# Kernel optimization log

Hardware: AMD Instinct MI355X
Metric: run time of the kernel (lower is better)

The kernel has to match this reference:

```python
import jax, jax.numpy as jnp
import numpy as np

EMBED_DIM = 1024
NUM_HEADS = 16
HEAD_DIM = EMBED_DIM // NUM_HEADS


def setup_inputs() -> dict:
    key = jax.random.key(0)
    ks = jax.random.split(key, 6)
    B, S = 2, 2048
    x = jax.random.normal(ks[0], (B, S, EMBED_DIM), dtype=jnp.float32)
    # causal boolean mask, broadcast to (B, H, S, S)
    causal = jnp.tril(jnp.ones((S, S), dtype=bool))
    mask = jnp.broadcast_to(causal, (B, NUM_HEADS, S, S))
    s_in = 1.0 / np.sqrt(EMBED_DIM)
    qkv_w = jax.random.normal(ks[1], (3 * EMBED_DIM, EMBED_DIM), dtype=jnp.float32) * s_in
    qkv_b = jax.random.normal(ks[2], (3 * EMBED_DIM,), dtype=jnp.float32) * 0.01
    proj_w = jax.random.normal(ks[3], (EMBED_DIM, EMBED_DIM), dtype=jnp.float32) * s_in
    proj_b = jax.random.normal(ks[4], (EMBED_DIM,), dtype=jnp.float32) * 0.01
    return {"x": x, "mask": mask, "qkv_w": qkv_w, "qkv_b": qkv_b,
            "proj_w": proj_w, "proj_b": proj_b}


def reference(x, mask, qkv_w, qkv_b, proj_w, proj_b):
    B, S, E = x.shape
    H, D = NUM_HEADS, HEAD_DIM
    qkv = x @ qkv_w.T + qkv_b                     # (B, S, 3E)
    q, k, v = jnp.split(qkv, 3, axis=-1)
    # (B, H, S, D)
    q = q.reshape(B, S, H, D).transpose(0, 2, 1, 3)
    k = k.reshape(B, S, H, D).transpose(0, 2, 1, 3)
    v = v.reshape(B, S, H, D).transpose(0, 2, 1, 3)
    scale = D ** (-0.5)
    attn = jnp.einsum('bhqd,bhkd->bhqk', q, k) * scale
    attn = jnp.where(mask, attn, jnp.float32(-10000.0))
    attn = attn - jnp.max(attn, axis=-1, keepdims=True)
    attn = jax.nn.softmax(attn, axis=-1)
    attn = jnp.where(mask, attn, jnp.float32(0.0))
    # dropout is identity in eval mode
    out = jnp.einsum('bhqk,bhkd->bhqd', attn, v)
    out = out.transpose(0, 2, 1, 3).reshape(B, S, E)
    return out @ proj_w.T + proj_b
```

## Files before the change

### kernel.cpp

```cpp
#include <hip/hip_runtime.h>
#include <hip/hip_bf16.h>

#define BATCH 2
#define SEQ 2048
#define EMBED 1024
#define NHEADS 16
#define HDIM 64

typedef __hip_bfloat16 bf16;
typedef __attribute__((ext_vector_type(8))) short bf16x8;
typedef __attribute__((ext_vector_type(4))) short bf16x4;
typedef __attribute__((ext_vector_type(4))) float f32x4;

typedef const __attribute__((address_space(1))) void* gaddr_t;
typedef __attribute__((address_space(3))) void* laddr_t;

__device__ __forceinline__ bf16x8 lds_frag8(const bf16* p) {
    const bf16x4 a = *(const bf16x4*)p;
    const bf16x4 b = *(const bf16x4*)(p + 4);
    return __builtin_shufflevector(a, b, 0, 1, 2, 3, 4, 5, 6, 7);
}

__global__ __launch_bounds__(256)
void f2b_all(const float* __restrict__ s0, bf16* __restrict__ d0, int n0,
             const float* __restrict__ s1, bf16* __restrict__ d1, int n1,
             const float* __restrict__ s2, bf16* __restrict__ d2, int n2)
{
    int i = blockIdx.x * 256 + threadIdx.x;
    const float* s; bf16* d;
    if (i < n0)                { s = s0; d = d0; }
    else if ((i -= n0) < n1)   { s = s1; d = d1; }
    else if ((i -= n1) < n2)   { s = s2; d = d2; }
    else return;
    const float4 v = ((const float4*)s)[i];
    union { ushort4 u4; bf16 h[4]; } o;
    o.h[0] = __float2bfloat16(v.x);
    o.h[1] = __float2bfloat16(v.y);
    o.h[2] = __float2bfloat16(v.z);
    o.h[3] = __float2bfloat16(v.w);
    ((ushort4*)d)[i] = o.u4;
}

template<int MODE>
__global__ __launch_bounds__(256)
void gemm_bt(const bf16* __restrict__ A, const bf16* __restrict__ B,
             const float* __restrict__ bias, void* __restrict__ Cv,
             int M, int N, int K)
{
    __shared__ __align__(16) bf16 lA[128 * 32];
    __shared__ __align__(16) bf16 lB[128 * 32];
    const int tid  = threadIdx.x;
    const int bn   = blockIdx.x, bm = blockIdx.y;
    const int wave = tid >> 6, lane = tid & 63;
    const int wm   = (wave >> 1) << 6, wn = (wave & 1) << 6;
    const int quad = lane >> 4, l16 = lane & 15;

    f32x4 acc[4][4] = {};

    for (int kt = 0; kt < K; kt += 32) {
        __syncthreads();
        #pragma unroll
        for (int i = 0; i < 2; ++i) {
            const int c = tid + (i << 8);
            const int r = c >> 2, kc = (c & 3) << 3;
            const bf16* gA = A + (long)(bm * 128 + r) * K + (kt + kc);
            const bf16* gB = B + (long)(bn * 128 + r) * K + (kt + kc);
            __builtin_amdgcn_global_load_lds((gaddr_t)gA, (laddr_t)&lA[c << 3], 16, 0, 0);
            __builtin_amdgcn_global_load_lds((gaddr_t)gB, (laddr_t)&lB[c << 3], 16, 0, 0);
        }
        __syncthreads();

        bf16x8 af[4], bfr[4];
        #pragma unroll
        for (int t = 0; t < 4; ++t) {
            af[t]  = *(const bf16x8*)&lA[(wm + t * 16 + l16) * 32 + quad * 8];
            bfr[t] = *(const bf16x8*)&lB[(wn + t * 16 + l16) * 32 + quad * 8];
        }
        #pragma unroll
        for (int tm = 0; tm < 4; ++tm)
            #pragma unroll
            for (int tn = 0; tn < 4; ++tn)
                acc[tm][tn] = __builtin_amdgcn_mfma_f32_16x16x32_bf16(
                    af[tm], bfr[tn], acc[tm][tn], 0, 0, 0);
    }

    #pragma unroll
    for (int tm = 0; tm < 4; ++tm) {
        #pragma unroll
        for (int tn = 0; tn < 4; ++tn) {
            const int gn = bn * 128 + wn + tn * 16 + l16;
            const float bv = bias[gn];
            if (MODE == 0) {
                #pragma unroll
                for (int r = 0; r < 4; ++r) {
                    const int gm = bm * 128 + wm + tm * 16 + quad * 4 + r;
                    ((float*)Cv)[(long)gm * N + gn] = acc[tm][tn][r] + bv;
                }
            } else {
                const int part = gn >> 10, h = (gn >> 6) & (NHEADS - 1), d = gn & (HDIM - 1);
                const int gm0 = bm * 128 + wm + tm * 16 + quad * 4;
                const int b = gm0 >> 11, s0 = gm0 & (SEQ - 1);
                if (part == 2) {
                    union { ushort4 u4; bf16 hv[4]; } o;
                    #pragma unroll
                    for (int r = 0; r < 4; ++r) o.hv[r] = __float2bfloat16(acc[tm][tn][r] + bv);
                    const long off = ((((long)2 * BATCH + b) * NHEADS + h) * HDIM + d) * SEQ + s0;
                    *(ushort4*)((bf16*)Cv + off) = o.u4;
                } else {
                    #pragma unroll
                    for (int r = 0; r < 4; ++r) {
                        const long off = ((((long)part * BATCH + b) * NHEADS + h) * SEQ + (s0 + r)) * HDIM + d;
                        ((bf16*)Cv)[off] = __float2bfloat16(acc[tm][tn][r] + bv);
                    }
                }
            }
        }
    }
}

__global__ __launch_bounds__(256)
void attn_nf(const bf16* __restrict__ Q, const bf16* __restrict__ K,
             const bf16* __restrict__ Vt, float* __restrict__ Op,
             float* __restrict__ lp)
{
    __shared__ __align__(16) bf16 pS[4 * 32 * 68];

    const int tid  = threadIdx.x;
    const int wave = tid >> 6, lane = tid & 63;
    const int quad = lane >> 4, l15 = lane & 15;
    const int bh   = blockIdx.x;
    const int half = blockIdx.y >> 4;
    const int qidx = blockIdx.y & 15;
    const int qg   = (15 - qidx) * 4 + wave;
    const int qw0  = qg * 32;

    const bf16* Qb  = Q  + (long)bh * SEQ * HDIM;
    const bf16* Kb  = K  + (long)bh * SEQ * HDIM;
    const bf16* Vtb = Vt + (long)bh * HDIM * SEQ;
    bf16* pW = pS + wave * 32 * 68;

    bf16x8 qf[2][2];
    #pragma unroll
    for (int mt = 0; mt < 2; ++mt)
        #pragma unroll
        for (int c = 0; c < 2; ++c) {
            union { int4 i; bf16x8 v; } u;
            u.i = *(const int4*)(Qb + (long)(qw0 + mt * 16 + l15) * HDIM + c * 32 + quad * 8);
            qf[mt][c] = u.v;
        }

    f32x4 acc[2][4] = {};
    float lsum[8] = {};

    const int nkt = (qw0 >> 6) + 1;
    const float sc = 0.125f * 1.44269504088896340736f;

    for (int t = half; t < nkt; t += 2) {
        const int kb = t * 64;

        f32x4 s[2][4] = {};
        #pragma unroll
        for (int c = 0; c < 2; ++c) {
            #pragma unroll
            for (int nt = 0; nt < 4; ++nt) {
                union { int4 i; bf16x8 v; } u;
                u.i = *(const int4*)(Kb + (long)(kb + nt * 16 + l15) * HDIM + c * 32 + quad * 8);
                #pragma unroll
                for (int mt = 0; mt < 2; ++mt)
                    s[mt][nt] = __builtin_amdgcn_mfma_f32_16x16x32_bf16(
                        qf[mt][c], u.v, s[mt][nt], 0, 0, 0);
            }
        }

        #pragma unroll
        for (int mt = 0; mt < 2; ++mt)
            #pragma unroll
            for (int nt = 0; nt < 4; ++nt)
                #pragma unroll
                for (int r = 0; r < 4; ++r) {
                    const int rl = mt * 16 + quad * 4 + r;
                    const int cl = nt * 16 + l15;
                    const float p = ((kb + cl) <= (qw0 + rl))
                        ? __builtin_amdgcn_exp2f(s[mt][nt][r] * sc) : 0.f;
                    lsum[mt * 4 + r] += p;
                    pW[rl * 68 + cl] = __float2bfloat16(p);
                }

        #pragma unroll
        for (int c = 0; c < 2; ++c) {
            bf16x8 pf[2];
            #pragma unroll
            for (int mt = 0; mt < 2; ++mt)
                pf[mt] = lds_frag8(&pW[(mt * 16 + l15) * 68 + c * 32 + quad * 8]);
            #pragma unroll
            for (int nt = 0; nt < 4; ++nt) {
                union { int4 i; bf16x8 v; } u;
                u.i = *(const int4*)(Vtb + (long)(nt * 16 + l15) * SEQ + kb + c * 32 + quad * 8);
                #pragma unroll
                for (int mt = 0; mt < 2; ++mt)
                    acc[mt][nt] = __builtin_amdgcn_mfma_f32_16x16x32_bf16(
                        pf[mt], u.v, acc[mt][nt], 0, 0, 0);
            }
        }
    }

    #pragma unroll
    for (int i = 0; i < 8; ++i)
        #pragma unroll
        for (int m = 1; m < 16; m <<= 1) lsum[i] += __shfl_xor(lsum[i], m, 64);

    const long halfO = (long)BATCH * NHEADS * SEQ * HDIM;
    float* Oh = Op + half * halfO + ((long)bh * SEQ) * HDIM;
    float* lh = lp + half * (BATCH * NHEADS * SEQ) + bh * SEQ;
    #pragma unroll
    for (int mt = 0; mt < 2; ++mt)
        #pragma unroll
        for (int r = 0; r < 4; ++r) {
            const int rl = mt * 16 + quad * 4 + r;
            float* orow = Oh + (long)(qw0 + rl) * HDIM;
            #pragma unroll
            for (int nt = 0; nt < 4; ++nt)
                orow[nt * 16 + l15] = acc[mt][nt][r];
            if (l15 == 0) lh[qw0 + rl] = lsum[mt * 4 + r];
        }
}

__global__ __launch_bounds__(256)
void attn_combine(const float* __restrict__ Op, const float* __restrict__ lp,
                  bf16* __restrict__ att)
{
    const int i = blockIdx.x * 256 + threadIdx.x;
    const int d4 = i & 15, q = (i >> 4) & (SEQ - 1), bh = i >> 15;
    const long halfO = (long)BATCH * NHEADS * SEQ * HDIM;
    const long rowo  = ((long)bh * SEQ + q) * HDIM;
    const float4 a = ((const float4*)(Op + rowo))[d4];
    const float4 b = ((const float4*)(Op + halfO + rowo))[d4];
    const int li = bh * SEQ + q;
    const float inv = 1.f / (lp[li] + lp[BATCH * NHEADS * SEQ + li]);
    const int bb = bh >> 4, h = bh & 15;
    union { ushort4 u4; bf16 hv[4]; } o;
    o.hv[0] = __float2bfloat16((a.x + b.x) * inv);
    o.hv[1] = __float2bfloat16((a.y + b.y) * inv);
    o.hv[2] = __float2bfloat16((a.z + b.z) * inv);
    o.hv[3] = __float2bfloat16((a.w + b.w) * inv);
    *(ushort4*)(att + ((long)bb * SEQ + q) * EMBED + h * HDIM + d4 * 4) = o.u4;
}

extern "C" void kernel_launch(void* const* d_in, const int* in_sizes, int n_in,
                              void* d_out, int out_size, void* d_ws, size_t ws_size,
                              hipStream_t stream)
{
    const float* x      = (const float*)d_in[0];
    const float* qkv_w  = (const float*)d_in[2];
    const float* qkv_b  = (const float*)d_in[3];
    const float* proj_w = (const float*)d_in[4];
    const float* proj_b = (const float*)d_in[5];
    float* out = (float*)d_out;

    const long nX  = (long)BATCH * SEQ * EMBED;
    const long nQW = 3L * EMBED * EMBED;
    const long nPW = (long)EMBED * EMBED;
    const long per = (long)BATCH * NHEADS * SEQ * HDIM;

    bf16* xw  = (bf16*)d_ws;
    bf16* qwm = xw + nX;
    bf16* pwm = qwm + nQW;
    bf16* qw  = pwm + nPW;
    bf16* kw  = qw + per;
    bf16* vw  = kw + per;
    bf16* att = vw + per;
    float* Op = (float*)(att + per);
    float* lp = Op + 2 * per;

    const int n0 = (int)(nX / 4), n1 = (int)(nQW / 4), n2 = (int)(nPW / 4);
    f2b_all<<<(n0 + n1 + n2 + 255) / 256, 256, 0, stream>>>(
        x, xw, n0, qkv_w, qwm, n1, proj_w, pwm, n2);

    gemm_bt<1><<<dim3(3 * EMBED / 128, BATCH * SEQ / 128), 256, 0, stream>>>(
        xw, qwm, qkv_b, qw, BATCH * SEQ, 3 * EMBED, EMBED);

    attn_nf<<<dim3(BATCH * NHEADS, 32), 256, 0, stream>>>(qw, kw, vw, Op, lp);
    attn_combine<<<(int)(per / 4 / 256), 256, 0, stream>>>(Op, lp, att);

    gemm_bt<0><<<dim3(EMBED / 128, BATCH * SEQ / 128), 256, 0, stream>>>(
        att, pwm, proj_b, out, BATCH * SEQ, EMBED, EMBED);
}
```

Before: 725.4 us.

## Transpose attention score MFMA, vectorize P stores, skip off-diagonal masking, narrow proj GEMM tile

The attention kernel now computes S transposed (K as the A operand), so each lane holds four consecutive keys for one query row. That lets P be written to LDS as 8-byte vector stores with a padded stride of 72 and read back as aligned 16-byte loads. The row-sum reduction shrinks to two shuffles, and causal masking is applied only on the diagonal tile. MFMA sections are wrapped in s_setprio. Separately, the output projection GEMM is templated to a 64-wide N tile, doubling its block count to improve occupancy on a small grid.

```diff
diff --git a/kernel.cpp b/kernel.cpp
--- a/kernel.cpp
+++ b/kernel.cpp
@@ -9,17 +9,10 @@
 
 typedef __hip_bfloat16 bf16;
 typedef __attribute__((ext_vector_type(8))) short bf16x8;
-typedef __attribute__((ext_vector_type(4))) short bf16x4;
 typedef __attribute__((ext_vector_type(4))) float f32x4;
 
 typedef const __attribute__((address_space(1))) void* gaddr_t;
 typedef __attribute__((address_space(3))) void* laddr_t;
-
-__device__ __forceinline__ bf16x8 lds_frag8(const bf16* p) {
-    const bf16x4 a = *(const bf16x4*)p;
-    const bf16x4 b = *(const bf16x4*)(p + 4);
-    return __builtin_shufflevector(a, b, 0, 1, 2, 3, 4, 5, 6, 7);
-}
 
 __global__ __launch_bounds__(256)
 void f2b_all(const float* __restrict__ s0, bf16* __restrict__ d0, int n0,
@@ -41,21 +34,22 @@
     ((ushort4*)d)[i] = o.u4;
 }
 
-template<int MODE>
+template<int MODE, int NT>
 __global__ __launch_bounds__(256)
 void gemm_bt(const bf16* __restrict__ A, const bf16* __restrict__ B,
              const float* __restrict__ bias, void* __restrict__ Cv,
              int M, int N, int K)
 {
+    constexpr int BN = NT * 32;
     __shared__ __align__(16) bf16 lA[128 * 32];
-    __shared__ __align__(16) bf16 lB[128 * 32];
+    __shared__ __align__(16) bf16 lB[BN * 32];
     const int tid  = threadIdx.x;
     const int bn   = blockIdx.x, bm = blockIdx.y;
     const int wave = tid >> 6, lane = tid & 63;
-    const int wm   = (wave >> 1) << 6, wn = (wave & 1) << 6;
+    const int wm   = (wave >> 1) << 6, wn = (wave & 1) * (NT << 4);
     const int quad = lane >> 4, l16 = lane & 15;
 
-    f32x4 acc[4][4] = {};
+    f32x4 acc[4][NT] = {};
 
     for (int kt = 0; kt < K; kt += 32) {
         __syncthreads();
@@ -64,22 +58,25 @@
             const int c = tid + (i << 8);
             const int r = c >> 2, kc = (c & 3) << 3;
             const bf16* gA = A + (long)(bm * 128 + r) * K + (kt + kc);
-            const bf16* gB = B + (long)(bn * 128 + r) * K + (kt + kc);
             __builtin_amdgcn_global_load_lds((gaddr_t)gA, (laddr_t)&lA[c << 3], 16, 0, 0);
-            __builtin_amdgcn_global_load_lds((gaddr_t)gB, (laddr_t)&lB[c << 3], 16, 0, 0);
+            if (c < BN * 4) {
+                const bf16* gB = B + (long)(bn * BN + r) * K + (kt + kc);
+                __builtin_amdgcn_global_load_lds((gaddr_t)gB, (laddr_t)&lB[c << 3], 16, 0, 0);
+            }
         }
         __syncthreads();
 
-        bf16x8 af[4], bfr[4];
-        #pragma unroll
-        for (int t = 0; t < 4; ++t) {
+        bf16x8 af[4], bfr[NT];
+        #pragma unroll
+        for (int t = 0; t < 4; ++t)
             af[t]  = *(const bf16x8*)&lA[(wm + t * 16 + l16) * 32 + quad * 8];
+        #pragma unroll
+        for (int t = 0; t < NT; ++t)
             bfr[t] = *(const bf16x8*)&lB[(wn + t * 16 + l16) * 32 + quad * 8];
-        }
         #pragma unroll
         for (int tm = 0; tm < 4; ++tm)
             #pragma unroll
-            for (int tn = 0; tn < 4; ++tn)
+            for (int tn = 0; tn < NT; ++tn)
                 acc[tm][tn] = __builtin_amdgcn_mfma_f32_16x16x32_bf16(
                     af[tm], bfr[tn], acc[tm][tn], 0, 0, 0);
     }
@@ -87,8 +84,8 @@
     #pragma unroll
     for (int tm = 0; tm < 4; ++tm) {
         #pragma unroll
-        for (int tn = 0; tn < 4; ++tn) {
-            const int gn = bn * 128 + wn + tn * 16 + l16;
+        for (int tn = 0; tn < NT; ++tn) {
+            const int gn = bn * BN + wn + tn * 16 + l16;
             const float bv = bias[gn];
             if (MODE == 0) {
                 #pragma unroll
@@ -123,7 +120,7 @@
              const bf16* __restrict__ Vt, float* __restrict__ Op,
              float* __restrict__ lp)
 {
-    __shared__ __align__(16) bf16 pS[4 * 32 * 68];
+    __shared__ __align__(16) bf16 pS[4 * 32 * 72];
 
     const int tid  = threadIdx.x;
     const int wave = tid >> 6, lane = tid & 63;
@@ -137,7 +134,7 @@
     const bf16* Qb  = Q  + (long)bh * SEQ * HDIM;
     const bf16* Kb  = K  + (long)bh * SEQ * HDIM;
     const bf16* Vtb = Vt + (long)bh * HDIM * SEQ;
-    bf16* pW = pS + wave * 32 * 68;
+    bf16* pW = pS + wave * 32 * 72;
 
     bf16x8 qf[2][2];
     #pragma unroll
@@ -150,7 +147,7 @@
         }
 
     f32x4 acc[2][4] = {};
-    float lsum[8] = {};
+    float lsum[2] = {};
 
     const int nkt = (qw0 >> 6) + 1;
     const float sc = 0.125f * 1.44269504088896340736f;
@@ -165,55 +162,66 @@
             for (int nt = 0; nt < 4; ++nt) {
                 union { int4 i; bf16x8 v; } u;
                 u.i = *(const int4*)(Kb + (long)(kb + nt * 16 + l15) * HDIM + c * 32 + quad * 8);
+                __builtin_amdgcn_s_setprio(1);
                 #pragma unroll
                 for (int mt = 0; mt < 2; ++mt)
                     s[mt][nt] = __builtin_amdgcn_mfma_f32_16x16x32_bf16(
-                        qf[mt][c], u.v, s[mt][nt], 0, 0, 0);
-            }
-        }
-
+                        u.v, qf[mt][c], s[mt][nt], 0, 0, 0);
+                __builtin_amdgcn_s_setprio(0);
+            }
+        }
+
+        const bool diag = (t == nkt - 1);
         #pragma unroll
         for (int mt = 0; mt < 2; ++mt)
             #pragma unroll
-            for (int nt = 0; nt < 4; ++nt)
+            for (int nt = 0; nt < 4; ++nt) {
+                union { ushort4 u4; bf16 hv[4]; } o;
                 #pragma unroll
                 for (int r = 0; r < 4; ++r) {
-                    const int rl = mt * 16 + quad * 4 + r;
-                    const int cl = nt * 16 + l15;
-                    const float p = ((kb + cl) <= (qw0 + rl))
-                        ? __builtin_amdgcn_exp2f(s[mt][nt][r] * sc) : 0.f;
-                    lsum[mt * 4 + r] += p;
-                    pW[rl * 68 + cl] = __float2bfloat16(p);
+                    float p = __builtin_amdgcn_exp2f(s[mt][nt][r] * sc);
+                    if (diag) {
+                        const int key = nt * 16 + quad * 4 + r;
+                        const int qq  = mt * 16 + l15;
+                        if ((kb + key) > (qw0 + qq)) p = 0.f;
+                    }
+                    lsum[mt] += p;
+                    o.hv[r] = __float2bfloat16(p);
                 }
+                *(ushort4*)&pW[(mt * 16 + l15) * 72 + nt * 16 + quad * 4] = o.u4;
+            }
 
         #pragma unroll
         for (int c = 0; c < 2; ++c) {
             bf16x8 pf[2];
             #pragma unroll
             for (int mt = 0; mt < 2; ++mt)
-                pf[mt] = lds_frag8(&pW[(mt * 16 + l15) * 68 + c * 32 + quad * 8]);
+                pf[mt] = *(const bf16x8*)&pW[(mt * 16 + l15) * 72 + c * 32 + quad * 8];
             #pragma unroll
             for (int nt = 0; nt < 4; ++nt) {
                 union { int4 i; bf16x8 v; } u;
                 u.i = *(const int4*)(Vtb + (long)(nt * 16 + l15) * SEQ + kb + c * 32 + quad * 8);
+                __builtin_amdgcn_s_setprio(1);
                 #pragma unroll
                 for (int mt = 0; mt < 2; ++mt)
                     acc[mt][nt] = __builtin_amdgcn_mfma_f32_16x16x32_bf16(
                         pf[mt], u.v, acc[mt][nt], 0, 0, 0);
-            }
-        }
-    }
-
-    #pragma unroll
-    for (int i = 0; i < 8; ++i)
-        #pragma unroll
-        for (int m = 1; m < 16; m <<= 1) lsum[i] += __shfl_xor(lsum[i], m, 64);
+                __builtin_amdgcn_s_setprio(0);
+            }
+        }
+    }
+
+    #pragma unroll
+    for (int i = 0; i < 2; ++i) {
+        lsum[i] += __shfl_xor(lsum[i], 16, 64);
+        lsum[i] += __shfl_xor(lsum[i], 32, 64);
+    }
 
     const long halfO = (long)BATCH * NHEADS * SEQ * HDIM;
     float* Oh = Op + half * halfO + ((long)bh * SEQ) * HDIM;
     float* lh = lp + half * (BATCH * NHEADS * SEQ) + bh * SEQ;
     #pragma unroll
-    for (int mt = 0; mt < 2; ++mt)
+    for (int mt = 0; mt < 2; ++mt) {
         #pragma unroll
         for (int r = 0; r < 4; ++r) {
             const int rl = mt * 16 + quad * 4 + r;
@@ -221,8 +229,9 @@
             #pragma unroll
             for (int nt = 0; nt < 4; ++nt)
                 orow[nt * 16 + l15] = acc[mt][nt][r];
-            if (l15 == 0) lh[qw0 + rl] = lsum[mt * 4 + r];
-        }
+        }
+        if (quad == 0) lh[qw0 + mt * 16 + l15] = lsum[mt];
+    }
 }
 
 __global__ __launch_bounds__(256)
@@ -276,12 +285,12 @@
     f2b_all<<<(n0 + n1 + n2 + 255) / 256, 256, 0, stream>>>(
         x, xw, n0, qkv_w, qwm, n1, proj_w, pwm, n2);
 
-    gemm_bt<1><<<dim3(3 * EMBED / 128, BATCH * SEQ / 128), 256, 0, stream>>>(
+    gemm_bt<1, 4><<<dim3(3 * EMBED / 128, BATCH * SEQ / 128), 256, 0, stream>>>(
         xw, qwm, qkv_b, qw, BATCH * SEQ, 3 * EMBED, EMBED);
 
     attn_nf<<<dim3(BATCH * NHEADS, 32), 256, 0, stream>>>(qw, kw, vw, Op, lp);
     attn_combine<<<(int)(per / 4 / 256), 256, 0, stream>>>(Op, lp, att);
 
-    gemm_bt<0><<<dim3(EMBED / 128, BATCH * SEQ / 128), 256, 0, stream>>>(
+    gemm_bt<0, 2><<<dim3(EMBED / 64, BATCH * SEQ / 128), 256, 0, stream>>>(
         att, pwm, proj_b, out, BATCH * SEQ, EMBED, EMBED);
 }
```

Result: slower. 744.6 us (+2.6%).
